# Performance work log

Measured on AMD Instinct MI355X. Metric: run time of the kernel, lower is better.

## Reference

```python
import jax, jax.numpy as jnp
import numpy as np

N_NODES = 100000
N_EDGES = 200000
D_LAT = 64
D_ENC = 32
N_FEAT = 2  # output features 'p', 'q'
D_IN = 2 * D_LAT + D_LAT + D_ENC + D_ENC  # 256
D_HID = 64


def setup_inputs() -> dict:
    key = jax.random.key(0)
    ks = jax.random.split(key, 12)
    return {
        "edge_array": jax.random.normal(ks[0], (N_EDGES, 4), dtype=jnp.float32),
        "h_local": jax.random.normal(ks[1], (N_NODES, D_LAT), dtype=jnp.float32),
        "h_global": jax.random.normal(ks[2], (1, D_LAT), dtype=jnp.float32),
        "enc_local": jax.random.normal(ks[3], (N_EDGES, D_ENC), dtype=jnp.float32),
        "enc_global": jax.random.normal(ks[4], (1, D_ENC), dtype=jnp.float32),
        "W1": jax.random.normal(ks[5], (N_FEAT, D_IN, D_HID), dtype=jnp.float32) / np.sqrt(D_IN),
        "b1": jnp.zeros((N_FEAT, D_HID), dtype=jnp.float32),
        "W2": jax.random.normal(ks[6], (N_FEAT, D_HID, D_HID), dtype=jnp.float32) / np.sqrt(D_HID),
        "b2": jnp.zeros((N_FEAT, D_HID), dtype=jnp.float32),
        "W3": jax.random.normal(ks[7], (N_FEAT, D_HID, 1), dtype=jnp.float32) / np.sqrt(D_HID),
        "b3": jnp.zeros((N_FEAT, 1), dtype=jnp.float32),
        "addr_from": jax.random.randint(ks[8], (N_EDGES,), 0, N_NODES, dtype=jnp.int32),
        "addr_to": jax.random.randint(ks[9], (N_EDGES,), 0, N_NODES, dtype=jnp.int32),
    }


def reference(edge_array, h_local, h_global, enc_local, enc_global,
              W1, b1, W2, b2, W3, b3, addr_from, addr_to):
    n = enc_local.shape[0]
    # gather node latents per address (drop/fill-0 semantics for out-of-range)
    g_from = h_local.at[addr_from].get(mode='fill', fill_value=0.0)  # [n, D_LAT]
    g_to = h_local.at[addr_to].get(mode='fill', fill_value=0.0)      # [n, D_LAT]
    # concat: [latents..., h_global*ones, enc_local, enc_global*ones]
    x = jnp.concatenate([
        g_from, g_to,
        jnp.broadcast_to(h_global, (n, h_global.shape[1])),
        enc_local,
        jnp.broadcast_to(enc_global, (n, enc_global.shape[1])),
    ], axis=1)  # [n, D_IN]
    # stacked per-feature MLPs (one MLP per output feature)
    h1 = jax.nn.leaky_relu(jnp.einsum('ni,fio->fno', x, W1) + b1[:, None, :])
    h2 = jax.nn.leaky_relu(jnp.einsum('fni,fio->fno', h1, W2) + b2[:, None, :])
    out = (jnp.einsum('fni,fio->fno', h2, W3) + b3[:, None, :])[..., 0]  # [F, n]
    isnan_mask = jnp.isnan(edge_array[:, 0])
    return jnp.where(isnan_mask[None, :], jnp.nan, out)
```

## Files before the change

### kernel.cpp

```cpp
#include <hip/hip_runtime.h>


#define OFF_W1 0
#define OFF_W2 40960
#define OFF_B1 57344
#define OFF_B2 57856
#define OFF_W3 58368
#define OFF_B3 58880
#define OFF_EA0 59392
#define NWAVE 8
#define LDS_TOTAL 58944
#define PREP_W_BLOCKS 114

typedef __attribute__((ext_vector_type(8))) short bf16x8;
typedef __attribute__((ext_vector_type(4))) float f32x4;
typedef __attribute__((ext_vector_type(16))) float f32x16;

__device__ inline short f2bf(float f) {
    unsigned u = __builtin_bit_cast(unsigned, f);
    u += 0x7FFFu + ((u >> 16) & 1u);
    return (short)(u >> 16);
}

__device__ inline float4 ld4(const float* p, bool v) {
    if (v) return *(const float4*)p;
    return make_float4(0.f, 0.f, 0.f, 0.f);
}

__device__ inline unsigned cvt_pk(float lo, float hi) {
    unsigned r;
    asm("v_cvt_pk_bf16_f32 %0, %1, %2" : "=v"(r) : "v"(lo), "v"(hi));
    return r;
}

__device__ inline bf16x8 pack8(float4 a, float4 b) {
    union { bf16x8 v; unsigned u[4]; } r;
    r.u[0] = cvt_pk(a.x, a.y);
    r.u[1] = cvt_pk(a.z, a.w);
    r.u[2] = cvt_pk(b.x, b.y);
    r.u[3] = cvt_pk(b.z, b.w);
    return r.v;
}

__device__ inline float lrelu(float x) { return fmaxf(x, 0.01f * x); }

__global__ void prep_all(const float* __restrict__ W1, const float* __restrict__ b1,
                         const float* __restrict__ W2, const float* __restrict__ b2,
                         const float* __restrict__ W3, const float* __restrict__ b3,
                         const float* __restrict__ h_global, const float* __restrict__ enc_global,
                         const float* __restrict__ edge_array, const float* __restrict__ h_local,
                         int n_edges, int n8,
                         float* __restrict__ ea0, short* __restrict__ hbf,
                         char* __restrict__ ws) {
    int b = blockIdx.x;
    if (b >= PREP_W_BLOCKS) {
        int rb = b - PREP_W_BLOCKS;
        int eb = (n_edges + 255) >> 8;
        if (rb < eb) {
            int e = rb * 256 + threadIdx.x;
            if (e < n_edges) ea0[e] = ((const float4*)edge_array)[e].x;
        } else {
            int i = (rb - eb) * 256 + threadIdx.x;
            if (i < n8) {
                float4 a = ((const float4*)h_local)[2 * i];
                float4 c = ((const float4*)h_local)[2 * i + 1];
                ((bf16x8*)hbf)[i] = pack8(a, c);
            } else if (i < n8 + 8) {
                ((bf16x8*)hbf)[i] = (bf16x8){0, 0, 0, 0, 0, 0, 0, 0};
            }
        }
        return;
    }
    int idx = b * 256 + threadIdx.x;
    short* w1f = (short*)(ws + OFF_W1);
    short* w2f = (short*)(ws + OFF_W2);
    float* bp1 = (float*)(ws + OFF_B1);
    float* bp2 = (float*)(ws + OFF_B2);
    float* wp3 = (float*)(ws + OFF_W3);
    float* bp3 = (float*)(ws + OFF_B3);
    if (idx < 20480) {
        int f = idx / 10240, r0 = idx % 10240;
        int kk = r0 / 1024, r1 = r0 % 1024;
        int mm = r1 / 512,  r2 = r1 % 512;
        int l = r2 / 8,     j = r2 % 8;
        int kt = kk * 16 + (l >> 5) * 8 + j;
        int r = (kt < 128) ? kt : kt + 64;
        int c = mm * 32 + (l & 31);
        w1f[idx] = f2bf(W1[(f * 256 + r) * 64 + c]);
    } else if (idx < 28672) {
        int i2 = idx - 20480;
        int f = i2 / 4096, r0 = i2 % 4096;
        int kk2 = r0 / 1024, r1 = r0 % 1024;
        int mm = r1 / 512,  r2 = r1 % 512;
        int l = r2 / 8,     j = r2 % 8;
        int k = kk2 * 16 + (l >> 5) * 8 + j;
        int c = mm * 32 + (l & 31);
        w2f[i2] = f2bf(W2[(f * 64 + k) * 64 + c]);
    } else if (idx < 28800) {
        int i3 = idx - 28672; int f = i3 / 64, o = i3 % 64;
        float s = b1[f * 64 + o];
        for (int t = 0; t < 64; ++t) s += h_global[t] * W1[(f * 256 + 128 + t) * 64 + o];
        for (int t = 0; t < 32; ++t) s += enc_global[t] * W1[(f * 256 + 224 + t) * 64 + o];
        bp1[i3] = s;
    } else if (idx < 28928) {
        int i4 = idx - 28800; bp2[i4] = b2[i4];
    } else if (idx < 29056) {
        int i5 = idx - 28928; wp3[i5] = W3[i5];
    } else if (idx < 29058) {
        bp3[idx - 29056] = b3[idx - 29056];
    }
}

template<bool HBF>
__global__ __launch_bounds__(512, 4) void main_kernel(
        const float* __restrict__ h_local, const float* __restrict__ enc_local,
        const int* __restrict__ addr_from, const int* __restrict__ addr_to,
        const char* __restrict__ ws, const float* __restrict__ ea0,
        const short* __restrict__ hbf, float* __restrict__ out,
        int n_edges, int n_nodes) {
    __shared__ __align__(16) char lds[LDS_TOTAL];
    const int tid = threadIdx.x;
    const int lane = tid & 63, wave = tid >> 6;
    const int col = lane & 31, hi = lane >> 5;
    const int niters = (n_edges + 31) >> 5;
    const int stride = gridDim.x * NWAVE;

    int t = blockIdx.x * NWAVE + wave;
    bool valid = t < niters;
    int af = 0, at = 0;
    if (valid) {
        int ec0 = t * 32 + col; if (ec0 >= n_edges) ec0 = n_edges - 1;
        af = addr_from[ec0]; at = addr_to[ec0];
    }

    #pragma unroll
    for (int it = 0; it < 7; ++it)
        ((float4*)lds)[it * 512 + tid] = ((const float4*)ws)[it * 512 + tid];
    if (tid < 100)
        ((float4*)(lds + 57344))[tid] = ((const float4*)(ws + 57344))[tid];
    __syncthreads();

    const float b3v0 = ((const float*)(lds + OFF_B3))[0];
    const float b3v1 = ((const float*)(lds + OFF_B3))[1];

    while (valid) {
        int tb = t * 32;
        int ec = tb + col; if (ec >= n_edges) ec = n_edges - 1;

        bf16x8 a1[10];
        float4 e0, e1, e2, e3;
        float ea;
        if (HBF) {
            unsigned ra = (unsigned)af < (unsigned)n_nodes ? (unsigned)af : (unsigned)n_nodes;
            unsigned rt = (unsigned)at < (unsigned)n_nodes ? (unsigned)at : (unsigned)n_nodes;
            const short* pf = hbf + (size_t)ra * 64 + hi * 8;
            const short* pt = hbf + (size_t)rt * 64 + hi * 8;
            a1[0] = *(const bf16x8*)pf;        a1[1] = *(const bf16x8*)(pf + 16);
            a1[2] = *(const bf16x8*)(pf + 32); a1[3] = *(const bf16x8*)(pf + 48);
            a1[4] = *(const bf16x8*)pt;        a1[5] = *(const bf16x8*)(pt + 16);
            a1[6] = *(const bf16x8*)(pt + 32); a1[7] = *(const bf16x8*)(pt + 48);
            const float* pe = enc_local + (size_t)ec * 32 + hi * 8;
            e0 = *(const float4*)pe;        e1 = *(const float4*)(pe + 4);
            e2 = *(const float4*)(pe + 16); e3 = *(const float4*)(pe + 20);
            ea = ea0[ec];
        } else {
            bool afv = (unsigned)af < (unsigned)n_nodes;
            bool atv = (unsigned)at < (unsigned)n_nodes;
            const float* pf = h_local + (size_t)(afv ? af : 0) * 64 + hi * 8;
            const float* pt = h_local + (size_t)(atv ? at : 0) * 64 + hi * 8;
            #pragma unroll
            for (int kk = 0; kk < 4; ++kk) {
                a1[kk]     = pack8(ld4(pf + 16 * kk, afv), ld4(pf + 16 * kk + 4, afv));
                a1[kk + 4] = pack8(ld4(pt + 16 * kk, atv), ld4(pt + 16 * kk + 4, atv));
            }
            const float* pe = enc_local + (size_t)ec * 32 + hi * 8;
            e0 = *(const float4*)pe;        e1 = *(const float4*)(pe + 4);
            e2 = *(const float4*)(pe + 16); e3 = *(const float4*)(pe + 20);
            ea = ea0[ec];
        }

        int tn = t + stride;
        bool vnext = tn < niters;
        int af2 = 0, at2 = 0;
        if (vnext) {
            int ec2 = tn * 32 + col; if (ec2 >= n_edges) ec2 = n_edges - 1;
            af2 = addr_from[ec2]; at2 = addr_to[ec2];
        }

        a1[8] = pack8(e0, e1);
        a1[9] = pack8(e2, e3);

        #pragma unroll
        for (int f = 0; f < 2; ++f) {
            f32x16 acc[2];
            #pragma unroll
            for (int mm = 0; mm < 2; ++mm)
                #pragma unroll
                for (int q2 = 0; q2 < 4; ++q2) {
                    f32x4 v = *(const f32x4*)(lds + OFF_B1 + (f * 64 + mm * 32 + q2 * 8 + hi * 4) * 4);
                    acc[mm][q2 * 4 + 0] = v[0]; acc[mm][q2 * 4 + 1] = v[1];
                    acc[mm][q2 * 4 + 2] = v[2]; acc[mm][q2 * 4 + 3] = v[3];
                }
            #pragma unroll
            for (int kk = 0; kk < 10; ++kk)
                #pragma unroll
                for (int mm = 0; mm < 2; ++mm) {
                    bf16x8 w = *(const bf16x8*)(lds + OFF_W1 + (((f * 10 + kk) * 2 + mm) * 64 + lane) * 16);
                    acc[mm] = __builtin_amdgcn_mfma_f32_32x32x16_bf16(w, a1[kk], acc[mm], 0, 0, 0);
                }

            unsigned pk[2][8];
            #pragma unroll
            for (int mm = 0; mm < 2; ++mm)
                #pragma unroll
                for (int i = 0; i < 8; ++i)
                    pk[mm][i] = cvt_pk(lrelu(acc[mm][2 * i]), lrelu(acc[mm][2 * i + 1]));

            f32x16 acc2[2];
            #pragma unroll
            for (int mm = 0; mm < 2; ++mm)
                #pragma unroll
                for (int q2 = 0; q2 < 4; ++q2) {
                    f32x4 v = *(const f32x4*)(lds + OFF_B2 + (f * 64 + mm * 32 + q2 * 8 + hi * 4) * 4);
                    acc2[mm][q2 * 4 + 0] = v[0]; acc2[mm][q2 * 4 + 1] = v[1];
                    acc2[mm][q2 * 4 + 2] = v[2]; acc2[mm][q2 * 4 + 3] = v[3];
                }
            #pragma unroll
            for (int kk2 = 0; kk2 < 4; ++kk2) {
                const int ms = kk2 >> 1, c = (kk2 & 1) * 4;
                unsigned pass0 = hi ? pk[ms][c + 0] : pk[ms][c + 2];
                unsigned pass1 = hi ? pk[ms][c + 1] : pk[ms][c + 3];
                unsigned sw0 = (unsigned)__shfl_xor((int)pass0, 32, 64);
                unsigned sw1 = (unsigned)__shfl_xor((int)pass1, 32, 64);
                union { bf16x8 v; unsigned u[4]; } bb;
                bb.u[0] = hi ? sw0 : pk[ms][c + 0];
                bb.u[1] = hi ? sw1 : pk[ms][c + 1];
                bb.u[2] = hi ? pk[ms][c + 2] : sw0;
                bb.u[3] = hi ? pk[ms][c + 3] : sw1;
                #pragma unroll
                for (int mm = 0; mm < 2; ++mm) {
                    bf16x8 w = *(const bf16x8*)(lds + OFF_W2 + (((f * 4 + kk2) * 2 + mm) * 64 + lane) * 16);
                    acc2[mm] = __builtin_amdgcn_mfma_f32_32x32x16_bf16(w, bb.v, acc2[mm], 0, 0, 0);
                }
            }

            float p = 0.f;
            #pragma unroll
            for (int mm = 0; mm < 2; ++mm)
                #pragma unroll
                for (int q2 = 0; q2 < 4; ++q2) {
                    f32x4 wv = *(const f32x4*)(lds + OFF_W3 + (f * 64 + mm * 32 + q2 * 8 + hi * 4) * 4);
                    #pragma unroll
                    for (int j = 0; j < 4; ++j)
                        p = fmaf(lrelu(acc2[mm][q2 * 4 + j]), wv[j], p);
                }
            p += __shfl_xor(p, 32, 64);

            if (lane < 32) {
                int ee = tb + col;
                if (ee < n_edges) {
                    float val = p + (f == 0 ? b3v0 : b3v1);
                    if (__builtin_isnan(ea)) val = __builtin_nanf("");
                    out[f * n_edges + ee] = val;
                }
            }
        }

        t = tn; valid = vnext; af = af2; at = at2;
    }
}

extern "C" void kernel_launch(void* const* d_in, const int* in_sizes, int n_in,
                              void* d_out, int out_size, void* d_ws, size_t ws_size,
                              hipStream_t stream) {
    const float* edge_array = (const float*)d_in[0];
    const float* h_local    = (const float*)d_in[1];
    const float* h_global   = (const float*)d_in[2];
    const float* enc_local  = (const float*)d_in[3];
    const float* enc_global = (const float*)d_in[4];
    const float* W1 = (const float*)d_in[5];
    const float* b1 = (const float*)d_in[6];
    const float* W2 = (const float*)d_in[7];
    const float* b2 = (const float*)d_in[8];
    const float* W3 = (const float*)d_in[9];
    const float* b3 = (const float*)d_in[10];
    const int* addr_from = (const int*)d_in[11];
    const int* addr_to   = (const int*)d_in[12];
    int n_edges = in_sizes[11];
    int n_nodes = in_sizes[1] / 64;
    int n8 = n_nodes * 8;
    char* ws = (char*)d_ws;

    size_t off_ea0 = OFF_EA0;
    size_t off_hbf = (off_ea0 + (size_t)n_edges * 4 + 255) & ~(size_t)255;
    size_t need = off_hbf + (size_t)(n_nodes + 1) * 128;
    bool use_hbf = ws_size >= need;
    float* ea0 = (float*)(ws + off_ea0);
    short* hbf = (short*)(ws + off_hbf);

    int eb = (n_edges + 255) / 256;
    int hb = (n8 + 8 + 255) / 256;
    int prep_blocks = PREP_W_BLOCKS + eb + (use_hbf ? hb : 0);
    hipLaunchKernelGGL(prep_all, dim3(prep_blocks), dim3(256), 0, stream,
                       W1, b1, W2, b2, W3, b3, h_global, enc_global,
                       edge_array, h_local, n_edges, use_hbf ? n8 : 0, ea0, hbf, ws);

    int niters = (n_edges + 31) / 32;
    int nblk = 512;
    if (nblk * NWAVE > niters) nblk = (niters + NWAVE - 1) / NWAVE;
    if (use_hbf) {
        hipLaunchKernelGGL((main_kernel<true>), dim3(nblk), dim3(512), 0, stream,
                           h_local, enc_local, addr_from, addr_to,
                           ws, ea0, hbf, (float*)d_out, n_edges, n_nodes);
    } else {
        hipLaunchKernelGGL((main_kernel<false>), dim3(nblk), dim3(512), 0, stream,
                           h_local, enc_local, addr_from, addr_to,
                           ws, ea0, hbf, (float*)d_out, n_edges, n_nodes);
    }
}
```

Measured before the change: 35.75 us.

## Hold per-feature MLP weights in registers and split features across wave pairs

Each wave pair now splits the two output-feature MLPs, so a wave handles one feature and keeps its W1/W2 bf16 fragments in registers instead of re-reading them from LDS every tile. Biases are folded into the GEMMs through an extra constant-one k-fragment, which replaces the per-tile bias loads. The bf16 pre-conversion of h_local and the edge_array column extraction in the prep kernel are dropped, so gathers read fp32 directly and the prep pass shrinks. The cost is much higher register use (launch bounds lowered to 2), an extra MFMA step per layer, and duplicated gather traffic because both waves of a pair load the same edge inputs.

```diff
diff --git a/kernel.cpp b/kernel.cpp
--- a/kernel.cpp
+++ b/kernel.cpp
@@ -2,15 +2,11 @@
 
 
 #define OFF_W1 0
-#define OFF_W2 40960
-#define OFF_B1 57344
-#define OFF_B2 57856
-#define OFF_W3 58368
-#define OFF_B3 58880
-#define OFF_EA0 59392
+#define OFF_W2 45056
+#define OFF_W3 65536
+#define OFF_B3 66048
+#define WS_NEED 66056
 #define NWAVE 8
-#define LDS_TOTAL 58944
-#define PREP_W_BLOCKS 114
 
 typedef __attribute__((ext_vector_type(8))) short bf16x8;
 typedef __attribute__((ext_vector_type(4))) float f32x4;
@@ -44,229 +40,186 @@
 
 __device__ inline float lrelu(float x) { return fmaxf(x, 0.01f * x); }
 
-__global__ void prep_all(const float* __restrict__ W1, const float* __restrict__ b1,
-                         const float* __restrict__ W2, const float* __restrict__ b2,
-                         const float* __restrict__ W3, const float* __restrict__ b3,
-                         const float* __restrict__ h_global, const float* __restrict__ enc_global,
-                         const float* __restrict__ edge_array, const float* __restrict__ h_local,
-                         int n_edges, int n8,
-                         float* __restrict__ ea0, short* __restrict__ hbf,
-                         char* __restrict__ ws) {
-    int b = blockIdx.x;
-    if (b >= PREP_W_BLOCKS) {
-        int rb = b - PREP_W_BLOCKS;
-        int eb = (n_edges + 255) >> 8;
-        if (rb < eb) {
-            int e = rb * 256 + threadIdx.x;
-            if (e < n_edges) ea0[e] = ((const float4*)edge_array)[e].x;
-        } else {
-            int i = (rb - eb) * 256 + threadIdx.x;
-            if (i < n8) {
-                float4 a = ((const float4*)h_local)[2 * i];
-                float4 c = ((const float4*)h_local)[2 * i + 1];
-                ((bf16x8*)hbf)[i] = pack8(a, c);
-            } else if (i < n8 + 8) {
-                ((bf16x8*)hbf)[i] = (bf16x8){0, 0, 0, 0, 0, 0, 0, 0};
-            }
-        }
-        return;
-    }
-    int idx = b * 256 + threadIdx.x;
-    short* w1f = (short*)(ws + OFF_W1);
-    short* w2f = (short*)(ws + OFF_W2);
-    float* bp1 = (float*)(ws + OFF_B1);
-    float* bp2 = (float*)(ws + OFF_B2);
-    float* wp3 = (float*)(ws + OFF_W3);
-    float* bp3 = (float*)(ws + OFF_B3);
-    if (idx < 20480) {
-        int f = idx / 10240, r0 = idx % 10240;
-        int kk = r0 / 1024, r1 = r0 % 1024;
-        int mm = r1 / 512,  r2 = r1 % 512;
-        int l = r2 / 8,     j = r2 % 8;
+__global__ void prep_w(const float* __restrict__ W1, const float* __restrict__ b1,
+                       const float* __restrict__ W2, const float* __restrict__ b2,
+                       const float* __restrict__ W3, const float* __restrict__ b3,
+                       const float* __restrict__ h_global, const float* __restrict__ enc_global,
+                       char* __restrict__ ws) {
+    int idx = blockIdx.x * 256 + threadIdx.x;
+    if (idx < 22528) {
+        int f = idx / 11264, r0 = idx % 11264;
+        int r1 = r0 % 1024;
+        int l = (r1 % 512) / 8, j = r1 % 8;
+        int kk = r0 / 1024;
+        int mm = r1 / 512;
         int kt = kk * 16 + (l >> 5) * 8 + j;
-        int r = (kt < 128) ? kt : kt + 64;
-        int c = mm * 32 + (l & 31);
-        w1f[idx] = f2bf(W1[(f * 256 + r) * 64 + c]);
-    } else if (idx < 28672) {
-        int i2 = idx - 20480;
-        int f = i2 / 4096, r0 = i2 % 4096;
-        int kk2 = r0 / 1024, r1 = r0 % 1024;
-        int mm = r1 / 512,  r2 = r1 % 512;
-        int l = r2 / 8,     j = r2 % 8;
-        int k = kk2 * 16 + (l >> 5) * 8 + j;
-        int c = mm * 32 + (l & 31);
-        w2f[i2] = f2bf(W2[(f * 64 + k) * 64 + c]);
-    } else if (idx < 28800) {
-        int i3 = idx - 28672; int f = i3 / 64, o = i3 % 64;
-        float s = b1[f * 64 + o];
-        for (int t = 0; t < 64; ++t) s += h_global[t] * W1[(f * 256 + 128 + t) * 64 + o];
-        for (int t = 0; t < 32; ++t) s += enc_global[t] * W1[(f * 256 + 224 + t) * 64 + o];
-        bp1[i3] = s;
-    } else if (idx < 28928) {
-        int i4 = idx - 28800; bp2[i4] = b2[i4];
-    } else if (idx < 29056) {
-        int i5 = idx - 28928; wp3[i5] = W3[i5];
-    } else if (idx < 29058) {
-        bp3[idx - 29056] = b3[idx - 29056];
-    }
-}
-
-template<bool HBF>
-__global__ __launch_bounds__(512, 4) void main_kernel(
-        const float* __restrict__ h_local, const float* __restrict__ enc_local,
+        int out = mm * 32 + (l & 31);
+        float v;
+        if (kt < 128)       v = W1[(f * 256 + kt) * 64 + out];
+        else if (kt < 160)  v = W1[(f * 256 + kt + 64) * 64 + out];
+        else if (kt == 160) {
+            float s = b1[f * 64 + out];
+            for (int t = 0; t < 64; ++t) s += h_global[t] * W1[(f * 256 + 128 + t) * 64 + out];
+            for (int t = 0; t < 32; ++t) s += enc_global[t] * W1[(f * 256 + 224 + t) * 64 + out];
+            v = s;
+        } else v = 0.f;
+        ((short*)(ws + OFF_W1))[idx] = f2bf(v);
+    } else if (idx < 32768) {
+        int i2 = idx - 22528;
+        int f = i2 / 5120, r0 = i2 % 5120;
+        int r1 = r0 % 1024;
+        int l = (r1 % 512) / 8, j = r1 % 8;
+        int kk2 = r0 / 1024;
+        int mm = r1 / 512;
+        int k2 = kk2 * 16 + (l >> 5) * 8 + j;
+        int out = mm * 32 + (l & 31);
+        float v;
+        if (k2 < 64)       v = W2[(f * 64 + k2) * 64 + out];
+        else if (k2 == 64) v = b2[f * 64 + out];
+        else               v = 0.f;
+        ((short*)(ws + OFF_W2))[i2] = f2bf(v);
+    } else if (idx < 32896) {
+        int i = idx - 32768;
+        ((float*)(ws + OFF_W3))[i] = W3[i];
+    } else if (idx < 32898) {
+        ((float*)(ws + OFF_B3))[idx - 32896] = b3[idx - 32896];
+    }
+}
+
+__global__ __launch_bounds__(512, 2) void main_kernel(
+        const float* __restrict__ edge_array, const float* __restrict__ h_local,
+        const float* __restrict__ enc_local,
         const int* __restrict__ addr_from, const int* __restrict__ addr_to,
-        const char* __restrict__ ws, const float* __restrict__ ea0,
-        const short* __restrict__ hbf, float* __restrict__ out,
+        const char* __restrict__ ws, float* __restrict__ out,
         int n_edges, int n_nodes) {
-    __shared__ __align__(16) char lds[LDS_TOTAL];
+    __shared__ __align__(16) float w3s[130];
     const int tid = threadIdx.x;
     const int lane = tid & 63, wave = tid >> 6;
     const int col = lane & 31, hi = lane >> 5;
-    const int niters = (n_edges + 31) >> 5;
-    const int stride = gridDim.x * NWAVE;
-
-    int t = blockIdx.x * NWAVE + wave;
-    bool valid = t < niters;
+    const int f = wave & 1;
+    const int ntiles = (n_edges + 31) >> 5;
+    const int stride = (gridDim.x * NWAVE) >> 1;
+
+    if (tid < 130) w3s[tid] = ((const float*)(ws + OFF_W3))[tid];
+
+    bf16x8 w1r[22], w2r[10];
+    {
+        const char* b1p = ws + OFF_W1 + (size_t)f * 22 * 1024 + lane * 16;
+        #pragma unroll
+        for (int i = 0; i < 22; ++i) w1r[i] = *(const bf16x8*)(b1p + i * 1024);
+        const char* b2p = ws + OFF_W2 + (size_t)f * 10 * 1024 + lane * 16;
+        #pragma unroll
+        for (int i = 0; i < 10; ++i) w2r[i] = *(const bf16x8*)(b2p + i * 1024);
+    }
+    __syncthreads();
+    const float b3v = w3s[128 + f];
+
+    bf16x8 cfrag;
+    {
+        union { bf16x8 v; unsigned u[4]; } c;
+        c.u[0] = (hi == 0) ? 0x00003F80u : 0u;
+        c.u[1] = 0u; c.u[2] = 0u; c.u[3] = 0u;
+        cfrag = c.v;
+    }
+
+    int t = (blockIdx.x * NWAVE + wave) >> 1;
     int af = 0, at = 0;
-    if (valid) {
-        int ec0 = t * 32 + col; if (ec0 >= n_edges) ec0 = n_edges - 1;
-        af = addr_from[ec0]; at = addr_to[ec0];
-    }
-
-    #pragma unroll
-    for (int it = 0; it < 7; ++it)
-        ((float4*)lds)[it * 512 + tid] = ((const float4*)ws)[it * 512 + tid];
-    if (tid < 100)
-        ((float4*)(lds + 57344))[tid] = ((const float4*)(ws + 57344))[tid];
-    __syncthreads();
-
-    const float b3v0 = ((const float*)(lds + OFF_B3))[0];
-    const float b3v1 = ((const float*)(lds + OFF_B3))[1];
-
-    while (valid) {
+    if (t < ntiles) {
+        int e0 = t * 32 + col; if (e0 >= n_edges) e0 = n_edges - 1;
+        af = addr_from[e0]; at = addr_to[e0];
+    }
+
+    while (t < ntiles) {
         int tb = t * 32;
         int ec = tb + col; if (ec >= n_edges) ec = n_edges - 1;
 
-        bf16x8 a1[10];
-        float4 e0, e1, e2, e3;
-        float ea;
-        if (HBF) {
-            unsigned ra = (unsigned)af < (unsigned)n_nodes ? (unsigned)af : (unsigned)n_nodes;
-            unsigned rt = (unsigned)at < (unsigned)n_nodes ? (unsigned)at : (unsigned)n_nodes;
-            const short* pf = hbf + (size_t)ra * 64 + hi * 8;
-            const short* pt = hbf + (size_t)rt * 64 + hi * 8;
-            a1[0] = *(const bf16x8*)pf;        a1[1] = *(const bf16x8*)(pf + 16);
-            a1[2] = *(const bf16x8*)(pf + 32); a1[3] = *(const bf16x8*)(pf + 48);
-            a1[4] = *(const bf16x8*)pt;        a1[5] = *(const bf16x8*)(pt + 16);
-            a1[6] = *(const bf16x8*)(pt + 32); a1[7] = *(const bf16x8*)(pt + 48);
-            const float* pe = enc_local + (size_t)ec * 32 + hi * 8;
-            e0 = *(const float4*)pe;        e1 = *(const float4*)(pe + 4);
-            e2 = *(const float4*)(pe + 16); e3 = *(const float4*)(pe + 20);
-            ea = ea0[ec];
-        } else {
-            bool afv = (unsigned)af < (unsigned)n_nodes;
-            bool atv = (unsigned)at < (unsigned)n_nodes;
-            const float* pf = h_local + (size_t)(afv ? af : 0) * 64 + hi * 8;
-            const float* pt = h_local + (size_t)(atv ? at : 0) * 64 + hi * 8;
-            #pragma unroll
-            for (int kk = 0; kk < 4; ++kk) {
-                a1[kk]     = pack8(ld4(pf + 16 * kk, afv), ld4(pf + 16 * kk + 4, afv));
-                a1[kk + 4] = pack8(ld4(pt + 16 * kk, atv), ld4(pt + 16 * kk + 4, atv));
+        bool afv = (unsigned)af < (unsigned)n_nodes;
+        bool atv = (unsigned)at < (unsigned)n_nodes;
+        const float* pf = h_local + (size_t)(afv ? af : 0) * 64 + hi * 8;
+        const float* pt = h_local + (size_t)(atv ? at : 0) * 64 + hi * 8;
+        const float* pe = enc_local + (size_t)ec * 32 + hi * 8;
+        bf16x8 a1[11];
+        #pragma unroll
+        for (int kk = 0; kk < 4; ++kk) {
+            a1[kk]     = pack8(ld4(pf + 16 * kk, afv), ld4(pf + 16 * kk + 4, afv));
+            a1[kk + 4] = pack8(ld4(pt + 16 * kk, atv), ld4(pt + 16 * kk + 4, atv));
+        }
+        a1[8] = pack8(*(const float4*)pe,        *(const float4*)(pe + 4));
+        a1[9] = pack8(*(const float4*)(pe + 16), *(const float4*)(pe + 20));
+        a1[10] = cfrag;
+        float ea = edge_array[4 * (size_t)ec];
+
+        int tn = t + stride;
+        int af2 = 0, at2 = 0;
+        if (tn < ntiles) {
+            int e2 = tn * 32 + col; if (e2 >= n_edges) e2 = n_edges - 1;
+            af2 = addr_from[e2]; at2 = addr_to[e2];
+        }
+
+        f32x16 acc[2];
+        #pragma unroll
+        for (int mm = 0; mm < 2; ++mm)
+            #pragma unroll
+            for (int i = 0; i < 16; ++i) acc[mm][i] = 0.f;
+        #pragma unroll
+        for (int kk = 0; kk < 11; ++kk)
+            #pragma unroll
+            for (int mm = 0; mm < 2; ++mm)
+                acc[mm] = __builtin_amdgcn_mfma_f32_32x32x16_bf16(w1r[kk * 2 + mm], a1[kk], acc[mm], 0, 0, 0);
+
+        unsigned pk[2][8];
+        #pragma unroll
+        for (int mm = 0; mm < 2; ++mm)
+            #pragma unroll
+            for (int i = 0; i < 8; ++i)
+                pk[mm][i] = cvt_pk(lrelu(acc[mm][2 * i]), lrelu(acc[mm][2 * i + 1]));
+
+        #pragma unroll
+        for (int mm = 0; mm < 2; ++mm)
+            #pragma unroll
+            for (int i = 0; i < 16; ++i) acc[mm][i] = 0.f;
+        #pragma unroll
+        for (int kk2 = 0; kk2 < 4; ++kk2) {
+            const int ms = kk2 >> 1, c = (kk2 & 1) * 4;
+            unsigned pass0 = hi ? pk[ms][c + 0] : pk[ms][c + 2];
+            unsigned pass1 = hi ? pk[ms][c + 1] : pk[ms][c + 3];
+            unsigned sw0 = (unsigned)__shfl_xor((int)pass0, 32, 64);
+            unsigned sw1 = (unsigned)__shfl_xor((int)pass1, 32, 64);
+            union { bf16x8 v; unsigned u[4]; } bb;
+            bb.u[0] = hi ? sw0 : pk[ms][c + 0];
+            bb.u[1] = hi ? sw1 : pk[ms][c + 1];
+            bb.u[2] = hi ? pk[ms][c + 2] : sw0;
+            bb.u[3] = hi ? pk[ms][c + 3] : sw1;
+            #pragma unroll
+            for (int mm = 0; mm < 2; ++mm)
+                acc[mm] = __builtin_amdgcn_mfma_f32_32x32x16_bf16(w2r[kk2 * 2 + mm], bb.v, acc[mm], 0, 0, 0);
+        }
+        #pragma unroll
+        for (int mm = 0; mm < 2; ++mm)
+            acc[mm] = __builtin_amdgcn_mfma_f32_32x32x16_bf16(w2r[8 + mm], cfrag, acc[mm], 0, 0, 0);
+
+        float p = 0.f;
+        #pragma unroll
+        for (int mm = 0; mm < 2; ++mm)
+            #pragma unroll
+            for (int q2 = 0; q2 < 4; ++q2) {
+                f32x4 wv = *(const f32x4*)&w3s[f * 64 + mm * 32 + q2 * 8 + hi * 4];
+                #pragma unroll
+                for (int j = 0; j < 4; ++j)
+                    p = fmaf(lrelu(acc[mm][q2 * 4 + j]), wv[j], p);
             }
-            const float* pe = enc_local + (size_t)ec * 32 + hi * 8;
-            e0 = *(const float4*)pe;        e1 = *(const float4*)(pe + 4);
-            e2 = *(const float4*)(pe + 16); e3 = *(const float4*)(pe + 20);
-            ea = ea0[ec];
-        }
-
-        int tn = t + stride;
-        bool vnext = tn < niters;
-        int af2 = 0, at2 = 0;
-        if (vnext) {
-            int ec2 = tn * 32 + col; if (ec2 >= n_edges) ec2 = n_edges - 1;
-            af2 = addr_from[ec2]; at2 = addr_to[ec2];
-        }
-
-        a1[8] = pack8(e0, e1);
-        a1[9] = pack8(e2, e3);
-
-        #pragma unroll
-        for (int f = 0; f < 2; ++f) {
-            f32x16 acc[2];
-            #pragma unroll
-            for (int mm = 0; mm < 2; ++mm)
-                #pragma unroll
-                for (int q2 = 0; q2 < 4; ++q2) {
-                    f32x4 v = *(const f32x4*)(lds + OFF_B1 + (f * 64 + mm * 32 + q2 * 8 + hi * 4) * 4);
-                    acc[mm][q2 * 4 + 0] = v[0]; acc[mm][q2 * 4 + 1] = v[1];
-                    acc[mm][q2 * 4 + 2] = v[2]; acc[mm][q2 * 4 + 3] = v[3];
-                }
-            #pragma unroll
-            for (int kk = 0; kk < 10; ++kk)
-                #pragma unroll
-                for (int mm = 0; mm < 2; ++mm) {
-                    bf16x8 w = *(const bf16x8*)(lds + OFF_W1 + (((f * 10 + kk) * 2 + mm) * 64 + lane) * 16);
-                    acc[mm] = __builtin_amdgcn_mfma_f32_32x32x16_bf16(w, a1[kk], acc[mm], 0, 0, 0);
-                }
-
-            unsigned pk[2][8];
-            #pragma unroll
-            for (int mm = 0; mm < 2; ++mm)
-                #pragma unroll
-                for (int i = 0; i < 8; ++i)
-                    pk[mm][i] = cvt_pk(lrelu(acc[mm][2 * i]), lrelu(acc[mm][2 * i + 1]));
-
-            f32x16 acc2[2];
-            #pragma unroll
-            for (int mm = 0; mm < 2; ++mm)
-                #pragma unroll
-                for (int q2 = 0; q2 < 4; ++q2) {
-                    f32x4 v = *(const f32x4*)(lds + OFF_B2 + (f * 64 + mm * 32 + q2 * 8 + hi * 4) * 4);
-                    acc2[mm][q2 * 4 + 0] = v[0]; acc2[mm][q2 * 4 + 1] = v[1];
-                    acc2[mm][q2 * 4 + 2] = v[2]; acc2[mm][q2 * 4 + 3] = v[3];
-                }
-            #pragma unroll
-            for (int kk2 = 0; kk2 < 4; ++kk2) {
-                const int ms = kk2 >> 1, c = (kk2 & 1) * 4;
-                unsigned pass0 = hi ? pk[ms][c + 0] : pk[ms][c + 2];
-                unsigned pass1 = hi ? pk[ms][c + 1] : pk[ms][c + 3];
-                unsigned sw0 = (unsigned)__shfl_xor((int)pass0, 32, 64);
-                unsigned sw1 = (unsigned)__shfl_xor((int)pass1, 32, 64);
-                union { bf16x8 v; unsigned u[4]; } bb;
-                bb.u[0] = hi ? sw0 : pk[ms][c + 0];
-                bb.u[1] = hi ? sw1 : pk[ms][c + 1];
-                bb.u[2] = hi ? pk[ms][c + 2] : sw0;
-                bb.u[3] = hi ? pk[ms][c + 3] : sw1;
-                #pragma unroll
-                for (int mm = 0; mm < 2; ++mm) {
-                    bf16x8 w = *(const bf16x8*)(lds + OFF_W2 + (((f * 4 + kk2) * 2 + mm) * 64 + lane) * 16);
-                    acc2[mm] = __builtin_amdgcn_mfma_f32_32x32x16_bf16(w, bb.v, acc2[mm], 0, 0, 0);
-                }
+        p += __shfl_xor(p, 32, 64);
+
+        if (lane < 32) {
+            int ee = tb + col;
+            if (ee < n_edges) {
+                float val = p + b3v;
+                if (__builtin_isnan(ea)) val = __builtin_nanf("");
+                out[(size_t)f * n_edges + ee] = val;
             }
-
-            float p = 0.f;
-            #pragma unroll
-            for (int mm = 0; mm < 2; ++mm)
-                #pragma unroll
-                for (int q2 = 0; q2 < 4; ++q2) {
-                    f32x4 wv = *(const f32x4*)(lds + OFF_W3 + (f * 64 + mm * 32 + q2 * 8 + hi * 4) * 4);
-                    #pragma unroll
-                    for (int j = 0; j < 4; ++j)
-                        p = fmaf(lrelu(acc2[mm][q2 * 4 + j]), wv[j], p);
-                }
-            p += __shfl_xor(p, 32, 64);
-
-            if (lane < 32) {
-                int ee = tb + col;
-                if (ee < n_edges) {
-                    float val = p + (f == 0 ? b3v0 : b3v1);
-                    if (__builtin_isnan(ea)) val = __builtin_nanf("");
-                    out[f * n_edges + ee] = val;
-                }
-            }
-        }
-
-        t = tn; valid = vnext; af = af2; at = at2;
+        }
+
+        t = tn; af = af2; at = at2;
     }
 }
 
@@ -288,33 +241,16 @@
     const int* addr_to   = (const int*)d_in[12];
     int n_edges = in_sizes[11];
     int n_nodes = in_sizes[1] / 64;
-    int n8 = n_nodes * 8;
     char* ws = (char*)d_ws;
 
-    size_t off_ea0 = OFF_EA0;
-    size_t off_hbf = (off_ea0 + (size_t)n_edges * 4 + 255) & ~(size_t)255;
-    size_t need = off_hbf + (size_t)(n_nodes + 1) * 128;
-    bool use_hbf = ws_size >= need;
-    float* ea0 = (float*)(ws + off_ea0);
-    short* hbf = (short*)(ws + off_hbf);
-
-    int eb = (n_edges + 255) / 256;
-    int hb = (n8 + 8 + 255) / 256;
-    int prep_blocks = PREP_W_BLOCKS + eb + (use_hbf ? hb : 0);
-    hipLaunchKernelGGL(prep_all, dim3(prep_blocks), dim3(256), 0, stream,
-                       W1, b1, W2, b2, W3, b3, h_global, enc_global,
-                       edge_array, h_local, n_edges, use_hbf ? n8 : 0, ea0, hbf, ws);
-
-    int niters = (n_edges + 31) / 32;
-    int nblk = 512;
-    if (nblk * NWAVE > niters) nblk = (niters + NWAVE - 1) / NWAVE;
-    if (use_hbf) {
-        hipLaunchKernelGGL((main_kernel<true>), dim3(nblk), dim3(512), 0, stream,
-                           h_local, enc_local, addr_from, addr_to,
-                           ws, ea0, hbf, (float*)d_out, n_edges, n_nodes);
-    } else {
-        hipLaunchKernelGGL((main_kernel<false>), dim3(nblk), dim3(512), 0, stream,
-                           h_local, enc_local, addr_from, addr_to,
-                           ws, ea0, hbf, (float*)d_out, n_edges, n_nodes);
-    }
-}
+    hipLaunchKernelGGL(prep_w, dim3(129), dim3(256), 0, stream,
+                       W1, b1, W2, b2, W3, b3, h_global, enc_global, ws);
+
+    int ntiles = (n_edges + 31) / 32;
+    int nblk = 256;
+    int nwpairs = (ntiles < nblk * NWAVE / 2) ? ntiles : nblk * NWAVE / 2;
+    if (nwpairs < nblk * NWAVE / 2) nblk = (nwpairs * 2 + NWAVE - 1) / NWAVE;
+    hipLaunchKernelGGL(main_kernel, dim3(nblk), dim3(512), 0, stream,
+                       edge_array, h_local, enc_local, addr_from, addr_to,
+                       ws, (float*)d_out, n_edges, n_nodes);
+}
```

Result: slower. 51.49 us (+44.0%).
